# Optimization experiments

Measured on AMD Instinct MI355X. Metric: run time of the kernel, lower is better.

## Reference

```python
import jax, jax.numpy as jnp
import numpy as np

SPATIAL = (128, 128)
FFT_SIZE = (256, 256)  # 2 * spatial per dim
FFT_AXES = (-2, -1)


def setup_inputs() -> dict:
    key = jax.random.key(0)
    k1, k2, k3, k4 = jax.random.split(key, 4)
    B, C = 4, 256
    u = jax.random.normal(k1, (B, C, *SPATIAL), dtype=jnp.float32)
    k = jax.random.normal(k2, (C, 64, 64), dtype=jnp.float32)
    pregate = jax.random.uniform(k3, (B, C, *SPATIAL), dtype=jnp.float32)
    postgate = jax.random.uniform(k4, (B, C, *SPATIAL), dtype=jnp.float32)
    return {"u": u, "k": k, "pregate": pregate, "postgate": postgate}


def reference(u, k, pregate, postgate):
    # y = crop(IRFFT(RFFT(u * pregate) * RFFT(k))) * postgate
    u_work = u.astype(jnp.float32) * pregate.astype(jnp.float32)
    u_f = jnp.fft.rfftn(u_work, s=FFT_SIZE, axes=FFT_AXES)      # (B,C,256,129) complex
    k_f = jnp.fft.rfftn(k.astype(jnp.float32), s=FFT_SIZE, axes=FFT_AXES)  # (C,256,129)
    y_f = u_f * k_f[None]
    y = jnp.fft.irfftn(y_f, s=FFT_SIZE, axes=FFT_AXES)          # (B,C,256,256)
    H, W = u.shape[-2], u.shape[-1]
    y = y[..., :H, :W]
    y = y * postgate.astype(jnp.float32)
    return y.astype(u.dtype)
```

## Files before the change

### kernel.cpp

```cpp
#include <hip/hip_runtime.h>


typedef unsigned int uint32;
typedef short short8 __attribute__((ext_vector_type(8)));
typedef float float4v __attribute__((ext_vector_type(4)));
typedef uint32 uint4v __attribute__((ext_vector_type(4)));

__device__ __forceinline__ unsigned short f2bf(float f) {
    uint32 x = __float_as_uint(f);
    uint32 r = (x + 0x7fffu + ((x >> 16) & 1u)) >> 16;
    return (unsigned short)r;
}

#define XLS_PITCH 160
#define XLS_BYTES (128 * XLS_PITCH * 2)
#define KPAD_BYTES (65 * 72 * 2)
#define SMEM_BYTES (XLS_BYTES + KPAD_BYTES)

__global__ __launch_bounds__(256, 3)
void conv_mfma4(const float* __restrict__ u, const float* __restrict__ kk,
                const float* __restrict__ pregate, const float* __restrict__ postgate,
                float* __restrict__ out)
{
    extern __shared__ char smem[];
    unsigned short (*xls)[XLS_PITCH] = (unsigned short(*)[XLS_PITCH])smem;
    unsigned short (*kpad)[72] = (unsigned short(*)[72])(smem + XLS_BYTES);

    const int img = blockIdx.x;
    const int c   = img & 255;
    const int tid = threadIdx.x;

    const float* uimg = u        + (size_t)img * (128*128);
    const float* pimg = pregate  + (size_t)img * (128*128);
    const float* gimg = postgate + (size_t)img * (128*128);
    float*       oimg = out      + (size_t)img * (128*128);
    const float* kimg = kk       + (size_t)c   * (64*64);

    const uint4 z = make_uint4(0u,0u,0u,0u);
    if (tid < 9) ((uint4*)&kpad[0][0])[tid] = z;
    for (int t = tid; t < 512; t += 256) {
        int r = t >> 2, cc = 128 + ((t & 3) << 3);
        *(uint4*)&xls[r][cc] = z;
    }
    for (int t = tid; t < 128*16; t += 256) {
        int r = t >> 4, c8 = (t & 15) << 3;
        const float4 u0 = *(const float4*)(uimg + r*128 + c8);
        const float4 u1 = *(const float4*)(uimg + r*128 + c8 + 4);
        const float4 p0 = *(const float4*)(pimg + r*128 + c8);
        const float4 p1 = *(const float4*)(pimg + r*128 + c8 + 4);
        unsigned short h0 = f2bf(u0.x*p0.x), h1 = f2bf(u0.y*p0.y);
        unsigned short h2 = f2bf(u0.z*p0.z), h3 = f2bf(u0.w*p0.w);
        unsigned short h4 = f2bf(u1.x*p1.x), h5 = f2bf(u1.y*p1.y);
        unsigned short h6 = f2bf(u1.z*p1.z), h7 = f2bf(u1.w*p1.w);
        uint4 w;
        w.x = (uint32)h7 | ((uint32)h6 << 16);
        w.y = (uint32)h5 | ((uint32)h4 << 16);
        w.z = (uint32)h3 | ((uint32)h2 << 16);
        w.w = (uint32)h1 | ((uint32)h0 << 16);
        *(uint4*)&xls[r][120 - c8] = w;
    }
    for (int t = tid; t < 64*16; t += 256) {
        int p = t >> 4, c4 = (t & 15) << 2;
        const float4 kv = *(const float4*)(kimg + p*64 + c4);
        uint2 w;
        w.x = (uint32)f2bf(kv.x) | ((uint32)f2bf(kv.y) << 16);
        w.y = (uint32)f2bf(kv.z) | ((uint32)f2bf(kv.w) << 16);
        *(uint2*)&kpad[1 + p][c4] = w;
    }
    __syncthreads();

    const int wv   = tid >> 6;
    const int lane = tid & 63;
    const int jw = wv >> 1;
    const int iw = (wv & 1) ^ ((blockIdx.x >> 8) & 1);
    const int m    = lane & 15;
    const int quad = lane >> 4;
    const int i16  = iw << 4;

    const int c0    = 127 - (jw << 4) - m + (quad << 3);
    const uint32 sh = (uint32)((c0 & 1) << 4);
    const int bw3   = (c0 >> 1) - 48;
    const int rhi   = 111 + i16;

    const uint32* xls32 = (const uint32*)smem;

    float4v acc[4][4] = {};

#pragma unroll 1
    for (int r = 0; r <= rhi; ++r) {
        const uint32* row32 = xls32 + r*80 + bw3;
        uint32 dw[4][5];
#pragma unroll
        for (int w = 0; w < 4; ++w) {
            const int O = (3 - w) << 4;
            dw[w][0] = row32[O+0]; dw[w][1] = row32[O+1];
            dw[w][2] = row32[O+2]; dw[w][3] = row32[O+3];
            dw[w][4] = row32[O+4];
        }
        short8 av[4];
#pragma unroll
        for (int w = 0; w < 4; ++w) {
            uint4v f;
            f.x = __builtin_amdgcn_alignbit(dw[w][1], dw[w][0], sh);
            f.y = __builtin_amdgcn_alignbit(dw[w][2], dw[w][1], sh);
            f.z = __builtin_amdgcn_alignbit(dw[w][3], dw[w][2], sh);
            f.w = __builtin_amdgcn_alignbit(dw[w][4], dw[w][3], sh);
            av[w] = __builtin_bit_cast(short8, f);
        }

        const int t0 = i16 + m - r;
#pragma unroll
        for (int nt = 0; nt < 4; ++nt) {
            const int nb = (nt << 5) + i16;
            if (r < nb - 63 || r > nb + 15) continue;
            const int p   = t0 + (nt << 5);
            const int row = ((uint32)p < 64u) ? (p + 1) : 0;
            const short8 bv0 = *(const short8*)&kpad[row][quad << 3];
            const short8 bv1 = *(const short8*)&kpad[row][32 + (quad << 3)];
            acc[0][nt] = __builtin_amdgcn_mfma_f32_16x16x32_bf16(av[0], bv0, acc[0][nt], 0,0,0);
            acc[1][nt] = __builtin_amdgcn_mfma_f32_16x16x32_bf16(av[1], bv0, acc[1][nt], 0,0,0);
            acc[2][nt] = __builtin_amdgcn_mfma_f32_16x16x32_bf16(av[2], bv0, acc[2][nt], 0,0,0);
            acc[3][nt] = __builtin_amdgcn_mfma_f32_16x16x32_bf16(av[3], bv0, acc[3][nt], 0,0,0);
            acc[1][nt] = __builtin_amdgcn_mfma_f32_16x16x32_bf16(av[0], bv1, acc[1][nt], 0,0,0);
            acc[2][nt] = __builtin_amdgcn_mfma_f32_16x16x32_bf16(av[1], bv1, acc[2][nt], 0,0,0);
            acc[3][nt] = __builtin_amdgcn_mfma_f32_16x16x32_bf16(av[2], bv1, acc[3][nt], 0,0,0);
        }
    }

    __syncthreads();
    float (*bufE)[132] = (float(*)[132])smem;
#pragma unroll
    for (int h = 0; h < 2; ++h) {
#pragma unroll
        for (int ntl = 0; ntl < 2; ++ntl) {
            const int iloc = (ntl << 5) + i16 + m;
#pragma unroll
            for (int mt = 0; mt < 4; ++mt)
#pragma unroll
                for (int rg = 0; rg < 4; ++rg)
                    bufE[iloc][(mt << 5) + (jw << 4) + (quad << 2) + rg] =
                        acc[mt][(h << 1) + ntl][rg];
        }
        __syncthreads();
#pragma unroll 1
        for (int s = 0; s < 8; ++s) {
            int chunk = (s << 8) + tid;
            int row = chunk >> 5, c4 = (chunk & 31) << 2;
            float4 v = *(float4*)&bufE[row][c4];
            int gi = (h << 6) + row;
            const float4 g = *(const float4*)(gimg + gi*128 + c4);
            float4 o;
            o.x = v.x*g.x; o.y = v.y*g.y; o.z = v.z*g.z; o.w = v.w*g.w;
            *(float4*)(oimg + gi*128 + c4) = o;
        }
        __syncthreads();
    }
}

extern "C" void kernel_launch(void* const* d_in, const int* in_sizes, int n_in,
                              void* d_out, int out_size, void* d_ws, size_t ws_size,
                              hipStream_t stream) {
    const float* u    = (const float*)d_in[0];
    const float* k    = (const float*)d_in[1];
    const float* pre  = (const float*)d_in[2];
    const float* post = (const float*)d_in[3];
    float* out = (float*)d_out;

    conv_mfma4<<<dim3(1024), dim3(256), SMEM_BYTES, stream>>>(u, k, pre, post, out);
}
```

Before: 329.9 us.

## Shrink LDS footprint with unpadded XOR-swizzled kernel tile and register masking

Drops the zero-padding column region of the input tile and the zero row of the kernel tile in LDS. Out-of-range elements are now masked in registers instead: a lane mask on the first A fragment, and a conditional zero on the B fragment near the band edges. The kernel tile is XOR-swizzled to avoid bank conflicts. The smaller LDS footprint lets launch bounds ask for 4 blocks per CU instead of 3, in exchange for extra ALU masking work and more register pressure under the tighter bound.

```diff
diff --git a/kernel.cpp b/kernel.cpp
--- a/kernel.cpp
+++ b/kernel.cpp
@@ -12,19 +12,18 @@
     return (unsigned short)r;
 }
 
-#define XLS_PITCH 160
-#define XLS_BYTES (128 * XLS_PITCH * 2)
-#define KPAD_BYTES (65 * 72 * 2)
+#define XLS_BYTES (128 * 128 * 2)
+#define KPAD_BYTES (64 * 64 * 2)
 #define SMEM_BYTES (XLS_BYTES + KPAD_BYTES)
 
-__global__ __launch_bounds__(256, 3)
-void conv_mfma4(const float* __restrict__ u, const float* __restrict__ kk,
+__global__ __launch_bounds__(256, 4)
+void conv_mfma5(const float* __restrict__ u, const float* __restrict__ kk,
                 const float* __restrict__ pregate, const float* __restrict__ postgate,
                 float* __restrict__ out)
 {
     extern __shared__ char smem[];
-    unsigned short (*xls)[XLS_PITCH] = (unsigned short(*)[XLS_PITCH])smem;
-    unsigned short (*kpad)[72] = (unsigned short(*)[72])(smem + XLS_BYTES);
+    unsigned short (*xls)[128] = (unsigned short(*)[128])smem;
+    unsigned short (*kpad)[64] = (unsigned short(*)[64])(smem + XLS_BYTES);
 
     const int img = blockIdx.x;
     const int c   = img & 255;
@@ -36,12 +35,6 @@
     float*       oimg = out      + (size_t)img * (128*128);
     const float* kimg = kk       + (size_t)c   * (64*64);
 
-    const uint4 z = make_uint4(0u,0u,0u,0u);
-    if (tid < 9) ((uint4*)&kpad[0][0])[tid] = z;
-    for (int t = tid; t < 512; t += 256) {
-        int r = t >> 2, cc = 128 + ((t & 3) << 3);
-        *(uint4*)&xls[r][cc] = z;
-    }
     for (int t = tid; t < 128*16; t += 256) {
         int r = t >> 4, c8 = (t & 15) << 3;
         const float4 u0 = *(const float4*)(uimg + r*128 + c8);
@@ -65,7 +58,8 @@
         uint2 w;
         w.x = (uint32)f2bf(kv.x) | ((uint32)f2bf(kv.y) << 16);
         w.y = (uint32)f2bf(kv.z) | ((uint32)f2bf(kv.w) << 16);
-        *(uint2*)&kpad[1 + p][c4] = w;
+        int sc = (((c4 >> 3) ^ (p & 7)) << 3) | (c4 & 7);
+        *(uint2*)&kpad[p][sc] = w;
     }
     __syncthreads();
 
@@ -82,13 +76,21 @@
     const int bw3   = (c0 >> 1) - 48;
     const int rhi   = 111 + i16;
 
+    const int rem = 127 - c0;
+    uint4v amask;
+    amask.x = (rem >= 0 ? 0x0000FFFFu : 0u) | (rem >= 1 ? 0xFFFF0000u : 0u);
+    amask.y = (rem >= 2 ? 0x0000FFFFu : 0u) | (rem >= 3 ? 0xFFFF0000u : 0u);
+    amask.z = (rem >= 4 ? 0x0000FFFFu : 0u) | (rem >= 5 ? 0xFFFF0000u : 0u);
+    amask.w = (rem >= 6 ? 0x0000FFFFu : 0u) | (rem >= 7 ? 0xFFFF0000u : 0u);
+
     const uint32* xls32 = (const uint32*)smem;
+    const short8 kzero = {};
 
     float4v acc[4][4] = {};
 
 #pragma unroll 1
     for (int r = 0; r <= rhi; ++r) {
-        const uint32* row32 = xls32 + r*80 + bw3;
+        const uint32* row32 = xls32 + r*64 + bw3;
         uint32 dw[4][5];
 #pragma unroll
         for (int w = 0; w < 4; ++w) {
@@ -105,6 +107,10 @@
             f.y = __builtin_amdgcn_alignbit(dw[w][2], dw[w][1], sh);
             f.z = __builtin_amdgcn_alignbit(dw[w][3], dw[w][2], sh);
             f.w = __builtin_amdgcn_alignbit(dw[w][4], dw[w][3], sh);
+            if (w == 0) {
+                f.x &= amask.x; f.y &= amask.y;
+                f.z &= amask.z; f.w &= amask.w;
+            }
             av[w] = __builtin_bit_cast(short8, f);
         }
 
@@ -113,10 +119,16 @@
         for (int nt = 0; nt < 4; ++nt) {
             const int nb = (nt << 5) + i16;
             if (r < nb - 63 || r > nb + 15) continue;
-            const int p   = t0 + (nt << 5);
-            const int row = ((uint32)p < 64u) ? (p + 1) : 0;
-            const short8 bv0 = *(const short8*)&kpad[row][quad << 3];
-            const short8 bv1 = *(const short8*)&kpad[row][32 + (quad << 3)];
+            const int p  = t0 + (nt << 5);
+            const int pr = p & 63;
+            const int px = pr & 7;
+            short8 bv0 = *(const short8*)&kpad[pr][(quad ^ px) << 3];
+            short8 bv1 = *(const short8*)&kpad[pr][((4 + quad) ^ px) << 3];
+            if (r > nb || r < nb - 48) {
+                const bool keep = ((uint32)p < 64u);
+                bv0 = keep ? bv0 : kzero;
+                bv1 = keep ? bv1 : kzero;
+            }
             acc[0][nt] = __builtin_amdgcn_mfma_f32_16x16x32_bf16(av[0], bv0, acc[0][nt], 0,0,0);
             acc[1][nt] = __builtin_amdgcn_mfma_f32_16x16x32_bf16(av[1], bv0, acc[1][nt], 0,0,0);
             acc[2][nt] = __builtin_amdgcn_mfma_f32_16x16x32_bf16(av[2], bv0, acc[2][nt], 0,0,0);
@@ -166,5 +178,5 @@
     const float* post = (const float*)d_in[3];
     float* out = (float*)d_out;
 
-    conv_mfma4<<<dim3(1024), dim3(256), SMEM_BYTES, stream>>>(u, k, pre, post, out);
+    conv_mfma5<<<dim3(1024), dim3(256), SMEM_BYTES, stream>>>(u, k, pre, post, out);
 }
```

Result: faster. 316.4 us (-4.1%).
